# Optimization experiments

Measured on AMD Instinct MI355X. Metric: run time of the kernel, lower is better.

Reference implementation:

```python
import jax, jax.numpy as jnp
import numpy as np
from jax import lax


def _lstm(x, h, c, Wx, Wh, b):
    z = x @ Wx + h @ Wh + b  # [B, 4u]
    i, f, g, o = jnp.split(z, 4, axis=-1)
    c2 = jax.nn.sigmoid(f) * c + jax.nn.sigmoid(i) * jnp.tanh(g)
    h2 = jax.nn.sigmoid(o) * jnp.tanh(c2)
    return h2, c2


def setup_inputs() -> dict:
    key = jax.random.key(0)
    ks = jax.random.split(key, 16)
    B, Tenc, E = 32, 512, 512          # batch, encoder steps, encoder embed_dim
    NMEL, TDEC = 80, 400               # mel channels, decoder steps
    P, A, D, F, K = 256, 128, 1024, 32, 31  # prenet, att_dim, dec_rnn, loc filters, loc kernel
    s = 0.05
    w = lambda k, shp: jax.random.normal(k, shp, jnp.float32) * s
    return {
        "enc_out": jax.random.normal(ks[0], (B, Tenc, E), jnp.float32),
        "mel_gt": jax.random.normal(ks[1], (B, NMEL, TDEC), jnp.float32),
        "prenet_w1": w(ks[2], (NMEL, P)), "prenet_b1": jnp.zeros((P,), jnp.float32),
        "prenet_w2": w(ks[3], (P, P)), "prenet_b2": jnp.zeros((P,), jnp.float32),
        "att_rnn_wx": w(ks[4], (P + E, 4 * A)), "att_rnn_wh": w(ks[5], (A, 4 * A)),
        "att_rnn_b": jnp.zeros((4 * A,), jnp.float32),
        "Wq": w(ks[6], (A, A)), "Wmem": w(ks[7], (E, A)),
        "conv_w": w(ks[8], (K, 2, F)), "Wloc": w(ks[9], (F, A)), "v": w(ks[10], (A, 1)),
        "dec_rnn_wx": w(ks[11], (A + E, 4 * D)), "dec_rnn_wh": w(ks[12], (D, 4 * D)),
        "dec_rnn_b": jnp.zeros((4 * D,), jnp.float32),
        "gate_w": w(ks[13], (D + E, 1)), "gate_b": jnp.zeros((1,), jnp.float32),
    }


def reference(enc_out, mel_gt, prenet_w1, prenet_b1, prenet_w2, prenet_b2,
              att_rnn_wx, att_rnn_wh, att_rnn_b, Wq, Wmem, conv_w, Wloc, v,
              dec_rnn_wx, dec_rnn_wh, dec_rnn_b, gate_w, gate_b):
    B, Tenc, E = enc_out.shape
    NMEL, TDEC = mel_gt.shape[1], mel_gt.shape[2]
    A = Wq.shape[0]
    D = dec_rnn_wh.shape[0]
    # faithful to source: reshape (n_frames_per_step=1), then time-major, prepend zero frame
    mel = jnp.reshape(mel_gt, (B, TDEC, NMEL))
    mel = jnp.transpose(mel, (1, 0, 2))                      # [TDEC, B, NMEL]
    mel = jnp.concatenate([jnp.zeros((1, B, NMEL), mel.dtype), mel], 0)  # [TDEC+1, B, NMEL]
    # prenet: 2 relu Dense layers (dropout deterministic/off in reference)
    pre = jax.nn.relu(jax.nn.relu(mel @ prenet_w1 + prenet_b1) @ prenet_w2 + prenet_b2)
    W_enc = enc_out @ Wmem                                    # processed memory [B, Tenc, A]
    dn = ('NWC', 'WIO', 'NWC')

    def step(carry, mel_in):
        att_h, att_c, dec_h, dec_c, ctx, aw, awc = carry
        x = jnp.concatenate([mel_in, ctx], -1)
        att_h, att_c = _lstm(x, att_h, att_c, att_rnn_wx, att_rnn_wh, att_rnn_b)
        pq = att_h @ Wq                                       # [B, A]
        loc = jnp.stack([aw, awc], -1)                        # [B, Tenc, 2]
        loc = lax.conv_general_dilated(loc, conv_w, (1,), 'SAME', dimension_numbers=dn)
        e = jnp.tanh(pq[:, None, :] + loc @ Wloc + W_enc) @ v # [B, Tenc, 1]
        aw = jax.nn.softmax(e[..., 0], axis=-1)
        awc = awc + aw
        ctx = jnp.einsum('bt,bte->be', aw, enc_out)
        dec_in = jnp.concatenate([att_h, ctx], -1)
        dec_h, dec_c = _lstm(dec_in, dec_h, dec_c, dec_rnn_wx, dec_rnn_wh, dec_rnn_b)
        hc = jnp.concatenate([dec_h, ctx], -1)                # returned as 'mel_out' (source behavior)
        gate = hc @ gate_w + gate_b
        return (att_h, att_c, dec_h, dec_c, ctx, aw, awc), (hc, gate)

    z = lambda shp: jnp.zeros(shp, jnp.float32)
    carry0 = (z((B, A)), z((B, A)), z((B, D)), z((B, D)), z((B, E)), z((B, Tenc)), z((B, Tenc)))
    _, (mels, gates) = lax.scan(step, carry0, pre)
    return mels, gates
```

## Files before the change

kernel.cpp:

```cpp
#include <hip/hip_runtime.h>

typedef unsigned short u16;
typedef unsigned int   u32;

#define NB 256
#define NT 512
#define TSTEPS 401
#define GATE_OFF   19709952

#define BAR_REL   4096
#define BAR_L2C   4128
#define BAR_FULLC 4160
#define BAR_FULLF 4192

#define OFF_ATTH    8192
#define OFF_ATTC    16384
#define OFF_DECH    20480
#define OFF_DECC    86016
#define OFF_CTX     118784
#define OFF_AW      135168
#define OFF_AWC     151552
#define OFF_PSUM    167936
#define OFF_E       168192
#define OFF_LOCA    184576
#define OFF_WENC    2281728
#define OFF_H2B     4378880
#define NEED_BYTES  24085504
#define ZERO_BYTES  (OFF_PSUM * 4)

#define LOG2E 1.44269504088896340736f

struct KParams {
    const void *enc, *mel, *pw1, *pb1, *pw2, *pb2, *awx, *awh, *ab, *wq,
               *wmem, *convw, *wloc, *vv, *dwx, *dwh, *db, *gw, *gb;
    float* ws;
    float* out;
};

__device__ __forceinline__ float bf2f(u16 h) {
    return __uint_as_float(((u32)h) << 16);
}
__device__ __forceinline__ u16 f2bf(float f) {
    u32 u = __float_as_uint(f);
    u32 lsb = (u >> 16) & 1u;
    u += 0x7fffu + lsb;
    return (u16)(u >> 16);
}
template<bool F32>
__device__ __forceinline__ float LD(const void* q, int i) {
    if (F32) return ((const float*)q)[i];
    return bf2f(((const u16*)q)[i]);
}
template<bool F32>
__device__ __forceinline__ float NTLD(const void* q, int i) {
    if (F32) return __builtin_nontemporal_load((const float*)q + i);
    return bf2f(__builtin_nontemporal_load((const u16*)q + i));
}
__device__ __forceinline__ float fexp2_(float x) { return __builtin_amdgcn_exp2f(x); }
__device__ __forceinline__ float frcp_(float x)  { return __builtin_amdgcn_rcpf(x); }
__device__ __forceinline__ float sigm_(float x) {
    return frcp_(1.0f + fexp2_(-LOG2E * x));
}
__device__ __forceinline__ float tanh_(float x) {
    float e = fexp2_(2.0f * LOG2E * x);
    return 1.0f - 2.0f * frcp_(e + 1.0f);
}

__device__ __forceinline__ float CL(const float* p) {
    return __hip_atomic_load(p, __ATOMIC_RELAXED, __HIP_MEMORY_SCOPE_AGENT);
}
__device__ __forceinline__ void CS(float* p, float v) {
    __hip_atomic_store(p, v, __ATOMIC_RELAXED, __HIP_MEMORY_SCOPE_AGENT);
}

__device__ __forceinline__ void gbarT(u32* wsb, u32 g, int blk) {
    __syncthreads();
    const int lane = threadIdx.x;
    if (lane < 64) {
        if (lane == 0)
            __hip_atomic_store(&wsb[blk * 16], g, __ATOMIC_RELAXED,
                               __HIP_MEMORY_SCOPE_AGENT);
        if (blk < 8) {
            for (;;) {
                u32 v = __hip_atomic_load(&wsb[(blk + 8 * (lane & 31)) * 16],
                                          __ATOMIC_RELAXED, __HIP_MEMORY_SCOPE_AGENT);
                unsigned long long ok = __ballot(v >= g);
                if (ok == ~0ull) break;
                __builtin_amdgcn_s_sleep(1);
            }
            if (lane == 0) {
                u32 prev = __hip_atomic_fetch_add(&wsb[BAR_L2C], 1u,
                    __ATOMIC_RELAXED, __HIP_MEMORY_SCOPE_AGENT);
                if (prev + 1u == 8u * g)
                    __hip_atomic_store(&wsb[BAR_REL], g, __ATOMIC_RELAXED,
                                       __HIP_MEMORY_SCOPE_AGENT);
            }
        }
        if (lane == 0) {
            u32 n = 0;
            for (;;) {
                u32 r = ((++n & 4095u) == 0u)
                    ? __hip_atomic_load(&wsb[BAR_REL], __ATOMIC_ACQUIRE,
                                        __HIP_MEMORY_SCOPE_AGENT)
                    : __hip_atomic_load(&wsb[BAR_REL], __ATOMIC_RELAXED,
                                        __HIP_MEMORY_SCOPE_AGENT);
                if (r >= g) break;
                __builtin_amdgcn_s_sleep(2);
            }
        }
    }
    __syncthreads();
}

__device__ __forceinline__ void gbar_full(u32* wsb) {
    __syncthreads();
    if (threadIdx.x == 0) {
        u32 prev = __hip_atomic_fetch_add(&wsb[BAR_FULLC], 1u, __ATOMIC_ACQ_REL,
                                          __HIP_MEMORY_SCOPE_AGENT);
        if (prev + 1u == (u32)NB) {
            __hip_atomic_store(&wsb[BAR_FULLF], 1u, __ATOMIC_RELEASE,
                               __HIP_MEMORY_SCOPE_AGENT);
        } else {
            u32 r;
            do {
                __builtin_amdgcn_s_sleep(8);
                r = __hip_atomic_load(&wsb[BAR_FULLF], __ATOMIC_ACQUIRE,
                                      __HIP_MEMORY_SCOPE_AGENT);
            } while (r < 1u);
        }
    }
    __syncthreads();
}

template<bool F32>
__device__ void decoder_body(const KParams& p, float* sm) {
    const int tid = threadIdx.x;
    const int blk = blockIdx.x;
    float* ws = p.ws;
    u32* wsb = (u32*)ws;
    u16* h2b = (u16*)(ws + OFF_H2B);
    float* outp = p.out;

    for (int r = blk; r < 12832; r += NB) {
        const int t = r >> 5, bb = r & 31;
        if (tid < 80)
            sm[tid] = (t > 0) ? LD<F32>(p.mel, bb * 32000 + (t - 1) * 80 + tid) : 0.0f;
        __syncthreads();
        if (tid < 256) {
            float a = LD<F32>(p.pb1, tid);
            for (int k = 0; k < 80; ++k) a += sm[k] * LD<F32>(p.pw1, k * 256 + tid);
            sm[96 + tid] = a > 0.f ? a : 0.f;
        }
        __syncthreads();
        if (tid < 256) {
            float a = LD<F32>(p.pb2, tid);
            for (int k = 0; k < 256; ++k) a += sm[96 + k] * LD<F32>(p.pw2, k * 256 + tid);
            h2b[r * 256 + tid] = f2bf(a > 0.f ? a : 0.f);
        }
        __syncthreads();
    }
    for (int r = blk; r < 16384; r += NB) {
        const int bb = r >> 9, te = r & 511;
        sm[tid] = NTLD<F32>(p.enc, bb * 262144 + te * 512 + tid);
        __syncthreads();
        if (tid < 128) {
            float a = 0.0f;
            for (int k = 0; k < 512; ++k) a += sm[k] * LD<F32>(p.wmem, k * 128 + tid);
            ws[OFF_WENC + r * 128 + tid] = a;
        }
        __syncthreads();
    }
    gbar_full(wsb);

    u32 gen = 0;

    for (int t = 0; t < TSTEPS; ++t) {
        const int pn = t & 1, po = pn ^ 1;

        if (blk < 32) {
            const int b = blk;
            for (int i = tid; i < 896; i += NT) {
                float v;
                if (i < 256)      v = bf2f(h2b[(t * 32 + b) * 256 + i]);
                else if (i < 768) v = CL(ws + OFF_CTX + b * 512 + (i - 256));
                else              v = CL(ws + OFF_ATTH + po * 4096 + b * 128 + (i - 768));
                sm[i] = v;
            }
            __syncthreads();
            {
                const int j = tid;
                float z = LD<F32>(p.ab, j);
                const int k0 = b * 24;
#pragma unroll 16
                for (int k = k0; k < 768; ++k) z += sm[k] * LD<F32>(p.awx, k * 512 + j);
#pragma unroll 16
                for (int k = 0; k < k0; ++k)   z += sm[k] * LD<F32>(p.awx, k * 512 + j);
                const int k0h = b * 4;
#pragma unroll 16
                for (int k = k0h; k < 128; ++k) z += sm[768 + k] * LD<F32>(p.awh, k * 512 + j);
#pragma unroll 16
                for (int k = 0; k < k0h; ++k)   z += sm[768 + k] * LD<F32>(p.awh, k * 512 + j);
                sm[896 + j] = z;
            }
            __syncthreads();
            if (tid < 128) {
                const int u = tid;
                float zi = sm[896 + u];
                float zf = sm[896 + 128 + u];
                float zg = sm[896 + 256 + u];
                float zo = sm[896 + 384 + u];
                float co = ws[OFF_ATTC + b * 128 + u];
                float cn = sigm_(zf) * co + sigm_(zi) * tanh_(zg);
                float hn = sigm_(zo) * tanh_(cn);
                ws[OFF_ATTC + b * 128 + u] = cn;
                CS(ws + OFF_ATTH + pn * 4096 + b * 128 + u, hn);
            }
        } else if (blk < 96) {
            const int idx = blk - 32, b = idx >> 1, th = idx & 1, te0 = th * 256;
            float* CONVL = sm + 572;
            for (int i = tid; i < 286; i += NT) {
                int te = te0 - 15 + i;
                bool ok = (te >= 0) && (te < 512);
                sm[i]       = ok ? CL(ws + OFF_AW + b * 512 + te) : 0.0f;
                sm[286 + i] = ok ? CL(ws + OFF_AWC + b * 512 + te) : 0.0f;
            }
            __syncthreads();
            {
                const int te_l = tid & 255, rf = tid >> 8;
                for (int ff = 0; ff < 16; ++ff) {
                    const int f = rf * 16 + ff;
                    float acc = 0.0f;
#pragma unroll
                    for (int k = 0; k < 31; ++k)
                        acc += sm[te_l + k] * LD<F32>(p.convw, k * 64 + f)
                             + sm[286 + te_l + k] * LD<F32>(p.convw, k * 64 + 32 + f);
                    CONVL[f * 256 + te_l] = acc;
                }
            }
            __syncthreads();
            {
                const int a_l = tid & 127, tg = tid >> 7;
                float wl[32];
#pragma unroll
                for (int f = 0; f < 32; ++f) wl[f] = LD<F32>(p.wloc, f * 128 + a_l);
#pragma unroll 4
                for (int te_i = tg * 64; te_i < tg * 64 + 64; ++te_i) {
                    const int te = te0 + te_i;
                    float acc = __builtin_nontemporal_load(
                        ws + OFF_WENC + (b * 512 + te) * 128 + a_l);
#pragma unroll 8
                    for (int f = 0; f < 32; ++f) acc += CONVL[f * 256 + te_i] * wl[f];
                    CS(ws + OFF_LOCA + (b * 512 + te) * 128 + a_l, acc);
                }
            }
        } else if (blk < 128) {
            if (t > 0) {
                const int b = blk - 96;
                const float* dh = ws + OFF_DECH + po * 32768 + b * 1024;
                float pg = CL(dh + tid) * LD<F32>(p.gw, tid)
                         + CL(dh + 512 + tid) * LD<F32>(p.gw, 512 + tid)
                         + CL(ws + OFF_CTX + b * 512 + tid) * LD<F32>(p.gw, 1024 + tid);
#pragma unroll
                for (int o = 32; o > 0; o >>= 1) pg += __shfl_down(pg, o, 64);
                if ((tid & 63) == 0) sm[tid >> 6] = pg;
                __syncthreads();
                if (tid == 0) {
                    float s = LD<F32>(p.gb, 0);
#pragma unroll
                    for (int w = 0; w < 8; ++w) s += sm[w];
                    outp[GATE_OFF + (t - 1) * 32 + b] = s;
                }
            }
        }
        gbarT(wsb, ++gen, blk);

        {
            const int b = blk >> 3, tc = blk & 7, te0 = tc * 64;
            if (tid < 128) {
                sm[512 + tid] = CL(ws + OFF_ATTH + pn * 4096 + b * 128 + tid);
                sm[128 + tid] = LD<F32>(p.vv, tid);
            }
            __syncthreads();
            if (tid < 128) {
                float pq = 0.0f;
                const int k0 = b * 4;
#pragma unroll 8
                for (int k = k0; k < 128; ++k)
                    pq += sm[512 + k] * LD<F32>(p.wq, k * 128 + tid);
#pragma unroll 8
                for (int k = 0; k < k0; ++k)
                    pq += sm[512 + k] * LD<F32>(p.wq, k * 128 + tid);
                sm[tid] = pq;
            }
            __syncthreads();
            {
                const int te_l = tid >> 3, ag = tid & 7;
                const int te = te0 + te_l;
                const float* lb = ws + OFF_LOCA + (b * 512 + te) * 128;
                float part = 0.0f;
#pragma unroll 16
                for (int aa = 0; aa < 16; ++aa) {
                    int a = ag * 16 + aa;
                    part += tanh_(CL(lb + a) + sm[a]) * sm[128 + a];
                }
                sm[256 + te_l * 8 + ag] = part;
            }
            __syncthreads();
            if (tid < 64) {
                float e = 0.0f;
#pragma unroll
                for (int ag = 0; ag < 8; ++ag) e += sm[256 + tid * 8 + ag];
                float ex = fexp2_(LOG2E * e);
                CS(ws + OFF_E + b * 512 + te0 + tid, ex);
#pragma unroll
                for (int o = 32; o > 0; o >>= 1) ex += __shfl_down(ex, o, 64);
                if (tid == 0) CS(ws + OFF_PSUM + b * 8 + tc, ex);
            }
        }
        gbarT(wsb, ++gen, blk);

        {
            const int b = blk >> 3, dc = blk & 7, d0 = dc * 64;
            float den = 0.0f;
#pragma unroll
            for (int i = 0; i < 8; ++i) den += CL(ws + OFF_PSUM + b * 8 + i);
            const float rden = frcp_(den);
            sm[tid] = CL(ws + OFF_E + b * 512 + tid);
            __syncthreads();
            if (dc == 0) {
                float awv = sm[tid] * rden;
                CS(ws + OFF_AW + b * 512 + tid, awv);
                CS(ws + OFF_AWC + b * 512 + tid,
                   CL(ws + OFF_AWC + b * 512 + tid) + awv);
            }
            {
                const int tg = tid >> 6, d = tid & 63;
                float part = 0.0f;
#pragma unroll 16
                for (int tt = 0; tt < 64; ++tt) {
                    int te = tg * 64 + tt;
                    part += sm[te] * NTLD<F32>(p.enc, b * 262144 + te * 512 + d0 + d);
                }
                sm[512 + tg * 64 + d] = part;
            }
            __syncthreads();
            if (tid < 64) {
                float cr = 0.0f;
#pragma unroll
                for (int tg = 0; tg < 8; ++tg) cr += sm[512 + tg * 64 + tid];
                float cv = cr * rden;
                int d = d0 + tid;
                CS(ws + OFF_CTX + b * 512 + d, cv);
                outp[t * 49152 + b * 1536 + 1024 + d] = cv;
            }
        }
        gbarT(wsb, ++gen, blk);

        {
            const int b = blk >> 3, jc = blk & 7;
            for (int i = tid; i < 1664; i += NT) {
                float v;
                if (i < 128)      v = CL(ws + OFF_ATTH + pn * 4096 + b * 128 + i);
                else if (i < 640) v = CL(ws + OFF_CTX + b * 512 + (i - 128));
                else              v = CL(ws + OFF_DECH + po * 32768 + b * 1024 + (i - 640));
                sm[i] = v;
            }
            __syncthreads();
            {
                const int g = tid >> 7, ul = tid & 127;
                const int j = g * 1024 + jc * 128 + ul;
                float z = LD<F32>(p.db, j);
                const int k0x = b * 20;
#pragma unroll 8
                for (int k = k0x; k < 640; ++k) z += sm[k] * LD<F32>(p.dwx, k * 4096 + j);
#pragma unroll 8
                for (int k = 0; k < k0x; ++k)   z += sm[k] * LD<F32>(p.dwx, k * 4096 + j);
                const int k0h = b * 32;
#pragma unroll 8
                for (int k = k0h; k < 1024; ++k) z += sm[640 + k] * LD<F32>(p.dwh, k * 4096 + j);
#pragma unroll 8
                for (int k = 0; k < k0h; ++k)    z += sm[640 + k] * LD<F32>(p.dwh, k * 4096 + j);
                sm[1664 + tid] = z;
            }
            __syncthreads();
            if (tid < 128) {
                const int u = jc * 128 + tid;
                float zi = sm[1664 + tid];
                float zf = sm[1664 + 128 + tid];
                float zg = sm[1664 + 256 + tid];
                float zo = sm[1664 + 384 + tid];
                float co = ws[OFF_DECC + b * 1024 + u];
                float cn = sigm_(zf) * co + sigm_(zi) * tanh_(zg);
                float hn = sigm_(zo) * tanh_(cn);
                ws[OFF_DECC + b * 1024 + u] = cn;
                CS(ws + OFF_DECH + pn * 32768 + b * 1024 + u, hn);
                outp[t * 49152 + b * 1536 + u] = hn;
            }
        }
        gbarT(wsb, ++gen, blk);
    }

    if (blk < 32) {
        const int b = blk;
        const float* dh = ws + OFF_DECH + 0 * 32768 + b * 1024;
        float pg = CL(dh + tid) * LD<F32>(p.gw, tid)
                 + CL(dh + 512 + tid) * LD<F32>(p.gw, 512 + tid)
                 + CL(ws + OFF_CTX + b * 512 + tid) * LD<F32>(p.gw, 1024 + tid);
#pragma unroll
        for (int o = 32; o > 0; o >>= 1) pg += __shfl_down(pg, o, 64);
        if ((tid & 63) == 0) sm[tid >> 6] = pg;
        __syncthreads();
        if (tid == 0) {
            float s = LD<F32>(p.gb, 0);
#pragma unroll
            for (int w = 0; w < 8; ++w) s += sm[w];
            outp[GATE_OFF + 400 * 32 + b] = s;
        }
    }
}

__device__ __forceinline__ bool probe_f32(const void* enc) {
    const u16* e = (const u16*)enc;
    int cnt = 0;
    for (int i = 0; i < 64; ++i) {
        u16 v = e[2 * i];
        int ex = (v >> 7) & 0xFF;
        if (ex >= 112 && ex <= 135) ++cnt;
    }
    return cnt < 48;
}

__global__ __launch_bounds__(NT, 2) void tts_decoder(KParams p) {
    __shared__ float sm[9216];
    __shared__ int flag_sh;
    if (threadIdx.x == 0) flag_sh = probe_f32(p.enc) ? 1 : 0;
    __syncthreads();
    if (flag_sh) decoder_body<true>(p, sm);
    else         decoder_body<false>(p, sm);
}

__global__ void ws_too_small(float* out) {
    if (threadIdx.x == 0 && blockIdx.x == 0) out[0] = 12345.0f;
}

extern "C" void kernel_launch(void* const* d_in, const int* in_sizes, int n_in,
                              void* d_out, int out_size, void* d_ws, size_t ws_size,
                              hipStream_t stream) {
    (void)in_sizes; (void)n_in; (void)out_size;
    if (ws_size < (size_t)NEED_BYTES) {
        ws_too_small<<<dim3(1), dim3(64), 0, stream>>>((float*)d_out);
        return;
    }
    KParams p;
    p.enc   = d_in[0];
    p.mel   = d_in[1];
    p.pw1   = d_in[2];
    p.pb1   = d_in[3];
    p.pw2   = d_in[4];
    p.pb2   = d_in[5];
    p.awx   = d_in[6];
    p.awh   = d_in[7];
    p.ab    = d_in[8];
    p.wq    = d_in[9];
    p.wmem  = d_in[10];
    p.convw = d_in[11];
    p.wloc  = d_in[12];
    p.vv    = d_in[13];
    p.dwx   = d_in[14];
    p.dwh   = d_in[15];
    p.db    = d_in[16];
    p.gw    = d_in[17];
    p.gb    = d_in[18];
    p.ws    = (float*)d_ws;
    p.out   = (float*)d_out;

    hipMemsetAsync(d_ws, 0, ZERO_BYTES, stream);

    void* args[] = {&p};
    hipError_t err = hipLaunchCooperativeKernel((void*)tts_decoder, dim3(NB), dim3(NT),
                                                args, 0, stream);
    if (err != hipSuccess) {
        tts_decoder<<<dim3(NB), dim3(NT), 0, stream>>>(p);
    }
}
```

Before: 129.1 ms.

## Restructure LSTM GEMVs to batch 8 rows per block and fuse location conv into energy stage

The attention and decoder LSTM matvecs now give each block 8 batch rows and a 64-column slice of the weights, so every weight load is reused across 8 batch elements instead of one. Pre-activations are written to the workspace and the LSTM cell nonlinearity is deferred to the next phase (attention cell inside the energy blocks, decoder cell inside the gate blocks). This removes the separate location-conv/LOCA phase and its large global intermediate, because conv and Wloc projection are recomputed inline in the energy computation. Outputs use nontemporal stores, shared memory grows and the 2-blocks-per-CU launch bound is dropped. Redundant recomputation of the attention cell across 8 chunk blocks and heavier shared memory use are the trade-offs.

```diff
diff --git a/kernel.cpp b/kernel.cpp
--- a/kernel.cpp
+++ b/kernel.cpp
@@ -14,18 +14,19 @@
 #define BAR_FULLF 4192
 
 #define OFF_ATTH    8192
-#define OFF_ATTC    16384
-#define OFF_DECH    20480
-#define OFF_DECC    86016
-#define OFF_CTX     118784
-#define OFF_AW      135168
-#define OFF_AWC     151552
-#define OFF_PSUM    167936
-#define OFF_E       168192
-#define OFF_LOCA    184576
-#define OFF_WENC    2281728
-#define OFF_H2B     4378880
-#define NEED_BYTES  24085504
+#define OFF_ATTC    12288
+#define OFF_ZATT    20480
+#define OFF_DECH    36864
+#define OFF_DECC    69632
+#define OFF_ZDEC    102400
+#define OFF_CTX     233472
+#define OFF_AW      249856
+#define OFF_AWC     266240
+#define OFF_PSUM    282624
+#define OFF_E       282880
+#define OFF_WENC    299264
+#define OFF_H2B     2396416
+#define NEED_BYTES  16155648
 #define ZERO_BYTES  (OFF_PSUM * 4)
 
 #define LOG2E 1.44269504088896340736f
@@ -55,6 +56,9 @@
 __device__ __forceinline__ float NTLD(const void* q, int i) {
     if (F32) return __builtin_nontemporal_load((const float*)q + i);
     return bf2f(__builtin_nontemporal_load((const u16*)q + i));
+}
+__device__ __forceinline__ void NTST(float* q, float v) {
+    __builtin_nontemporal_store(v, q);
 }
 __device__ __forceinline__ float fexp2_(float x) { return __builtin_amdgcn_exp2f(x); }
 __device__ __forceinline__ float frcp_(float x)  { return __builtin_amdgcn_rcpf(x); }
@@ -178,88 +182,60 @@
         const int pn = t & 1, po = pn ^ 1;
 
         if (blk < 32) {
-            const int b = blk;
-            for (int i = tid; i < 896; i += NT) {
-                float v;
-                if (i < 256)      v = bf2f(h2b[(t * 32 + b) * 256 + i]);
-                else if (i < 768) v = CL(ws + OFF_CTX + b * 512 + (i - 256));
-                else              v = CL(ws + OFF_ATTH + po * 4096 + b * 128 + (i - 768));
-                sm[i] = v;
+            const int o = blk >> 3, cg = blk & 7;
+            const int b0 = o * 8, j0 = cg * 64;
+#pragma unroll
+            for (int w8 = 0; w8 < 8; ++w8) {
+                const int bb = b0 + w8;
+                float* xs = sm + w8 * 896;
+                for (int k = tid; k < 896; k += NT) {
+                    float v;
+                    if (k < 256)      v = bf2f(h2b[(t * 32 + bb) * 256 + k]);
+                    else if (k < 768) v = CL(ws + OFF_CTX + bb * 512 + (k - 256));
+                    else              v = CL(ws + OFF_ATTH + bb * 128 + (k - 768));
+                    xs[k] = v;
+                }
             }
             __syncthreads();
             {
-                const int j = tid;
+                const int w = tid >> 6, l = tid & 63, j = j0 + l;
+                const int bb = b0 + w;
+                const float* xs = sm + w * 896;
                 float z = LD<F32>(p.ab, j);
-                const int k0 = b * 24;
-#pragma unroll 16
-                for (int k = k0; k < 768; ++k) z += sm[k] * LD<F32>(p.awx, k * 512 + j);
-#pragma unroll 16
-                for (int k = 0; k < k0; ++k)   z += sm[k] * LD<F32>(p.awx, k * 512 + j);
-                const int k0h = b * 4;
-#pragma unroll 16
-                for (int k = k0h; k < 128; ++k) z += sm[768 + k] * LD<F32>(p.awh, k * 512 + j);
-#pragma unroll 16
-                for (int k = 0; k < k0h; ++k)   z += sm[768 + k] * LD<F32>(p.awh, k * 512 + j);
-                sm[896 + j] = z;
-            }
-            __syncthreads();
-            if (tid < 128) {
-                const int u = tid;
-                float zi = sm[896 + u];
-                float zf = sm[896 + 128 + u];
-                float zg = sm[896 + 256 + u];
-                float zo = sm[896 + 384 + u];
-                float co = ws[OFF_ATTC + b * 128 + u];
-                float cn = sigm_(zf) * co + sigm_(zi) * tanh_(zg);
-                float hn = sigm_(zo) * tanh_(cn);
-                ws[OFF_ATTC + b * 128 + u] = cn;
-                CS(ws + OFF_ATTH + pn * 4096 + b * 128 + u, hn);
-            }
-        } else if (blk < 96) {
-            const int idx = blk - 32, b = idx >> 1, th = idx & 1, te0 = th * 256;
-            float* CONVL = sm + 572;
-            for (int i = tid; i < 286; i += NT) {
-                int te = te0 - 15 + i;
-                bool ok = (te >= 0) && (te < 512);
-                sm[i]       = ok ? CL(ws + OFF_AW + b * 512 + te) : 0.0f;
-                sm[286 + i] = ok ? CL(ws + OFF_AWC + b * 512 + te) : 0.0f;
-            }
-            __syncthreads();
-            {
-                const int te_l = tid & 255, rf = tid >> 8;
-                for (int ff = 0; ff < 16; ++ff) {
-                    const int f = rf * 16 + ff;
-                    float acc = 0.0f;
-#pragma unroll
-                    for (int k = 0; k < 31; ++k)
-                        acc += sm[te_l + k] * LD<F32>(p.convw, k * 64 + f)
-                             + sm[286 + te_l + k] * LD<F32>(p.convw, k * 64 + 32 + f);
-                    CONVL[f * 256 + te_l] = acc;
-                }
-            }
-            __syncthreads();
-            {
-                const int a_l = tid & 127, tg = tid >> 7;
-                float wl[32];
-#pragma unroll
-                for (int f = 0; f < 32; ++f) wl[f] = LD<F32>(p.wloc, f * 128 + a_l);
-#pragma unroll 4
-                for (int te_i = tg * 64; te_i < tg * 64 + 64; ++te_i) {
-                    const int te = te0 + te_i;
-                    float acc = __builtin_nontemporal_load(
-                        ws + OFF_WENC + (b * 512 + te) * 128 + a_l);
-#pragma unroll 8
-                    for (int f = 0; f < 32; ++f) acc += CONVL[f * 256 + te_i] * wl[f];
-                    CS(ws + OFF_LOCA + (b * 512 + te) * 128 + a_l, acc);
-                }
-            }
-        } else if (blk < 128) {
+                const int k0 = o * 192;
+#pragma unroll 8
+                for (int k = k0; k < 768; ++k) z += xs[k] * LD<F32>(p.awx, k * 512 + j);
+#pragma unroll 8
+                for (int k = 0; k < k0; ++k)   z += xs[k] * LD<F32>(p.awx, k * 512 + j);
+                const int k0h = o * 32;
+#pragma unroll 8
+                for (int k = k0h; k < 128; ++k) z += xs[768 + k] * LD<F32>(p.awh, k * 512 + j);
+#pragma unroll 8
+                for (int k = 0; k < k0h; ++k)   z += xs[768 + k] * LD<F32>(p.awh, k * 512 + j);
+                CS(ws + OFF_ZATT + bb * 512 + j, z);
+            }
+        } else if (blk < 64) {
             if (t > 0) {
-                const int b = blk - 96;
-                const float* dh = ws + OFF_DECH + po * 32768 + b * 1024;
-                float pg = CL(dh + tid) * LD<F32>(p.gw, tid)
-                         + CL(dh + 512 + tid) * LD<F32>(p.gw, 512 + tid)
-                         + CL(ws + OFF_CTX + b * 512 + tid) * LD<F32>(p.gw, 1024 + tid);
+                const int bb = blk - 32;
+                float h0 = 0.0f, h1 = 0.0f;
+#pragma unroll
+                for (int r = 0; r < 2; ++r) {
+                    const int u = tid + r * 512;
+                    float zi = CL(ws + OFF_ZDEC + bb * 4096 + u);
+                    float zf = CL(ws + OFF_ZDEC + bb * 4096 + 1024 + u);
+                    float zg = CL(ws + OFF_ZDEC + bb * 4096 + 2048 + u);
+                    float zo = CL(ws + OFF_ZDEC + bb * 4096 + 3072 + u);
+                    float co = ws[OFF_DECC + bb * 1024 + u];
+                    float cn = sigm_(zf) * co + sigm_(zi) * tanh_(zg);
+                    float hn = sigm_(zo) * tanh_(cn);
+                    ws[OFF_DECC + bb * 1024 + u] = cn;
+                    CS(ws + OFF_DECH + bb * 1024 + u, hn);
+                    NTST(outp + (t - 1) * 49152 + bb * 1536 + u, hn);
+                    if (r == 0) h0 = hn; else h1 = hn;
+                }
+                float pg = h0 * LD<F32>(p.gw, tid)
+                         + h1 * LD<F32>(p.gw, 512 + tid)
+                         + CL(ws + OFF_CTX + bb * 512 + tid) * LD<F32>(p.gw, 1024 + tid);
 #pragma unroll
                 for (int o = 32; o > 0; o >>= 1) pg += __shfl_down(pg, o, 64);
                 if ((tid & 63) == 0) sm[tid >> 6] = pg;
@@ -268,7 +244,7 @@
                     float s = LD<F32>(p.gb, 0);
 #pragma unroll
                     for (int w = 0; w < 8; ++w) s += sm[w];
-                    outp[GATE_OFF + (t - 1) * 32 + b] = s;
+                    NTST(outp + GATE_OFF + (t - 1) * 32 + bb, s);
                 }
             }
         }
@@ -276,9 +252,40 @@
 
         {
             const int b = blk >> 3, tc = blk & 7, te0 = tc * 64;
+            sm[tid] = CL(ws + OFF_ZATT + b * 512 + tid);
+            if (tid < 188) {
+                const int half = tid >= 94, ii = tid - half * 94;
+                const int te = te0 - 15 + ii;
+                const bool ok = (te >= 0) && (te < 512);
+                float v = ok ? CL(ws + (half ? OFF_AWC : OFF_AW) + b * 512 + te) : 0.0f;
+                sm[896 + half * 96 + ii] = v;
+            }
+            __syncthreads();
             if (tid < 128) {
-                sm[512 + tid] = CL(ws + OFF_ATTH + pn * 4096 + b * 128 + tid);
-                sm[128 + tid] = LD<F32>(p.vv, tid);
+                const int u = tid;
+                float zi = sm[u], zf = sm[128 + u], zg = sm[256 + u], zo = sm[384 + u];
+                float co = CL(ws + OFF_ATTC + po * 4096 + b * 128 + u);
+                float cn = sigm_(zf) * co + sigm_(zi) * tanh_(zg);
+                float hn = sigm_(zo) * tanh_(cn);
+                sm[512 + u] = hn;
+                sm[768 + u] = LD<F32>(p.vv, u);
+                if (tc == 0) {
+                    CS(ws + OFF_ATTC + pn * 4096 + b * 128 + u, cn);
+                    CS(ws + OFF_ATTH + b * 128 + u, hn);
+                }
+            }
+            {
+                const int te_l = tid & 63, rf = tid >> 6;
+#pragma unroll
+                for (int ff = 0; ff < 4; ++ff) {
+                    const int f = rf * 4 + ff;
+                    float acc = 0.0f;
+#pragma unroll
+                    for (int k = 0; k < 31; ++k)
+                        acc += sm[896 + te_l + k] * LD<F32>(p.convw, k * 64 + f)
+                             + sm[992 + te_l + k] * LD<F32>(p.convw, k * 64 + 32 + f);
+                    sm[1088 + f * 64 + te_l] = acc;
+                }
             }
             __syncthreads();
             if (tid < 128) {
@@ -290,26 +297,30 @@
 #pragma unroll 8
                 for (int k = 0; k < k0; ++k)
                     pq += sm[512 + k] * LD<F32>(p.wq, k * 128 + tid);
-                sm[tid] = pq;
+                sm[640 + tid] = pq;
             }
             __syncthreads();
             {
                 const int te_l = tid >> 3, ag = tid & 7;
                 const int te = te0 + te_l;
-                const float* lb = ws + OFF_LOCA + (b * 512 + te) * 128;
+                const float* wb = ws + OFF_WENC + (b * 512 + te) * 128;
                 float part = 0.0f;
-#pragma unroll 16
+#pragma unroll 4
                 for (int aa = 0; aa < 16; ++aa) {
-                    int a = ag * 16 + aa;
-                    part += tanh_(CL(lb + a) + sm[a]) * sm[128 + a];
-                }
-                sm[256 + te_l * 8 + ag] = part;
+                    const int a = ag * 16 + aa;
+                    float loc = __builtin_nontemporal_load(wb + a);
+#pragma unroll 8
+                    for (int f = 0; f < 32; ++f)
+                        loc += sm[1088 + f * 64 + te_l] * LD<F32>(p.wloc, f * 128 + a);
+                    part += tanh_(loc + sm[640 + a]) * sm[768 + a];
+                }
+                sm[3136 + te_l * 8 + ag] = part;
             }
             __syncthreads();
             if (tid < 64) {
                 float e = 0.0f;
 #pragma unroll
-                for (int ag = 0; ag < 8; ++ag) e += sm[256 + tid * 8 + ag];
+                for (int ag = 0; ag < 8; ++ag) e += sm[3136 + tid * 8 + ag];
                 float ex = fexp2_(LOG2E * e);
                 CS(ws + OFF_E + b * 512 + te0 + tid, ex);
 #pragma unroll
@@ -351,61 +362,67 @@
                 float cv = cr * rden;
                 int d = d0 + tid;
                 CS(ws + OFF_CTX + b * 512 + d, cv);
-                outp[t * 49152 + b * 1536 + 1024 + d] = cv;
+                NTST(outp + t * 49152 + b * 1536 + 1024 + d, cv);
             }
         }
         gbarT(wsb, ++gen, blk);
 
         {
-            const int b = blk >> 3, jc = blk & 7;
-            for (int i = tid; i < 1664; i += NT) {
-                float v;
-                if (i < 128)      v = CL(ws + OFF_ATTH + pn * 4096 + b * 128 + i);
-                else if (i < 640) v = CL(ws + OFF_CTX + b * 512 + (i - 128));
-                else              v = CL(ws + OFF_DECH + po * 32768 + b * 1024 + (i - 640));
-                sm[i] = v;
+            const int o = blk >> 6, cg = blk & 63;
+            const int b0 = o * 8, j0 = cg * 64;
+#pragma unroll
+            for (int w8 = 0; w8 < 8; ++w8) {
+                const int bb = b0 + w8;
+                float* xs = sm + w8 * 1664;
+                for (int k = tid; k < 1664; k += NT) {
+                    float v;
+                    if (k < 128)      v = CL(ws + OFF_ATTH + bb * 128 + k);
+                    else if (k < 640) v = CL(ws + OFF_CTX + bb * 512 + (k - 128));
+                    else              v = CL(ws + OFF_DECH + bb * 1024 + (k - 640));
+                    xs[k] = v;
+                }
             }
             __syncthreads();
             {
-                const int g = tid >> 7, ul = tid & 127;
-                const int j = g * 1024 + jc * 128 + ul;
+                const int w = tid >> 6, l = tid & 63, j = j0 + l;
+                const int bb = b0 + w;
+                const float* xs = sm + w * 1664;
                 float z = LD<F32>(p.db, j);
-                const int k0x = b * 20;
-#pragma unroll 8
-                for (int k = k0x; k < 640; ++k) z += sm[k] * LD<F32>(p.dwx, k * 4096 + j);
-#pragma unroll 8
-                for (int k = 0; k < k0x; ++k)   z += sm[k] * LD<F32>(p.dwx, k * 4096 + j);
-                const int k0h = b * 32;
-#pragma unroll 8
-                for (int k = k0h; k < 1024; ++k) z += sm[640 + k] * LD<F32>(p.dwh, k * 4096 + j);
-#pragma unroll 8
-                for (int k = 0; k < k0h; ++k)    z += sm[640 + k] * LD<F32>(p.dwh, k * 4096 + j);
-                sm[1664 + tid] = z;
-            }
-            __syncthreads();
-            if (tid < 128) {
-                const int u = jc * 128 + tid;
-                float zi = sm[1664 + tid];
-                float zf = sm[1664 + 128 + tid];
-                float zg = sm[1664 + 256 + tid];
-                float zo = sm[1664 + 384 + tid];
-                float co = ws[OFF_DECC + b * 1024 + u];
-                float cn = sigm_(zf) * co + sigm_(zi) * tanh_(zg);
-                float hn = sigm_(zo) * tanh_(cn);
-                ws[OFF_DECC + b * 1024 + u] = cn;
-                CS(ws + OFF_DECH + pn * 32768 + b * 1024 + u, hn);
-                outp[t * 49152 + b * 1536 + u] = hn;
+                const int k0x = o * 160;
+#pragma unroll 8
+                for (int k = k0x; k < 640; ++k) z += xs[k] * LD<F32>(p.dwx, k * 4096 + j);
+#pragma unroll 8
+                for (int k = 0; k < k0x; ++k)   z += xs[k] * LD<F32>(p.dwx, k * 4096 + j);
+                const int k0h = o * 256;
+#pragma unroll 8
+                for (int k = k0h; k < 1024; ++k) z += xs[640 + k] * LD<F32>(p.dwh, k * 4096 + j);
+#pragma unroll 8
+                for (int k = 0; k < k0h; ++k)    z += xs[640 + k] * LD<F32>(p.dwh, k * 4096 + j);
+                CS(ws + OFF_ZDEC + bb * 4096 + j, z);
             }
         }
         gbarT(wsb, ++gen, blk);
     }
 
-    if (blk < 32) {
-        const int b = blk;
-        const float* dh = ws + OFF_DECH + 0 * 32768 + b * 1024;
-        float pg = CL(dh + tid) * LD<F32>(p.gw, tid)
-                 + CL(dh + 512 + tid) * LD<F32>(p.gw, 512 + tid)
-                 + CL(ws + OFF_CTX + b * 512 + tid) * LD<F32>(p.gw, 1024 + tid);
+    if (blk >= 32 && blk < 64) {
+        const int bb = blk - 32;
+        float h0 = 0.0f, h1 = 0.0f;
+#pragma unroll
+        for (int r = 0; r < 2; ++r) {
+            const int u = tid + r * 512;
+            float zi = CL(ws + OFF_ZDEC + bb * 4096 + u);
+            float zf = CL(ws + OFF_ZDEC + bb * 4096 + 1024 + u);
+            float zg = CL(ws + OFF_ZDEC + bb * 4096 + 2048 + u);
+            float zo = CL(ws + OFF_ZDEC + bb * 4096 + 3072 + u);
+            float co = ws[OFF_DECC + bb * 1024 + u];
+            float cn = sigm_(zf) * co + sigm_(zi) * tanh_(zg);
+            float hn = sigm_(zo) * tanh_(cn);
+            NTST(outp + 400 * 49152 + bb * 1536 + u, hn);
+            if (r == 0) h0 = hn; else h1 = hn;
+        }
+        float pg = h0 * LD<F32>(p.gw, tid)
+                 + h1 * LD<F32>(p.gw, 512 + tid)
+                 + CL(ws + OFF_CTX + bb * 512 + tid) * LD<F32>(p.gw, 1024 + tid);
 #pragma unroll
         for (int o = 32; o > 0; o >>= 1) pg += __shfl_down(pg, o, 64);
         if ((tid & 63) == 0) sm[tid >> 6] = pg;
@@ -414,7 +431,7 @@
             float s = LD<F32>(p.gb, 0);
 #pragma unroll
             for (int w = 0; w < 8; ++w) s += sm[w];
-            outp[GATE_OFF + 400 * 32 + b] = s;
+            NTST(outp + GATE_OFF + 400 * 32 + bb, s);
         }
     }
 }
@@ -430,8 +447,8 @@
     return cnt < 48;
 }
 
-__global__ __launch_bounds__(NT, 2) void tts_decoder(KParams p) {
-    __shared__ float sm[9216];
+__global__ __launch_bounds__(NT) void tts_decoder(KParams p) {
+    __shared__ float sm[13312];
     __shared__ int flag_sh;
     if (threadIdx.x == 0) flag_sh = probe_f32(p.enc) ? 1 : 0;
     __syncthreads();
```

Measured after the change: 179.7 ms. 39.1% more time.
